# Optimization experiments

Measured on AMD Instinct MI355X. Metric: run time of the kernel, lower is better.

The kernel has to match this reference:

```python
import jax, jax.numpy as jnp
import numpy as np

N_NODES = 8192
N_EDGES = 262144
IN_DIM = 256
HID = 256
OUT_DIM = 64
PATH_DIM = 64
N_HEADS = 4


def setup_inputs() -> dict:
    key = jax.random.key(0)
    ks = jax.random.split(key, 16)
    s = 0.05
    x = jax.random.normal(ks[0], (N_NODES, IN_DIM), dtype=jnp.float32)
    edge_index = jax.random.randint(ks[1], (2, N_EDGES), 0, N_NODES, dtype=jnp.int32)
    return {
        "x": x,
        "edge_index": edge_index,
        # pathway encoder Linear(IN_DIM, PATH_DIM)
        "pe_w": jax.random.normal(ks[2], (IN_DIM, PATH_DIM), jnp.float32) * s,
        "pe_b": jax.random.normal(ks[3], (PATH_DIM,), jnp.float32) * s,
        # MultiheadAttention packed in-proj [3E, E] and out-proj [E, E]
        "in_proj_w": jax.random.normal(ks[4], (3 * PATH_DIM, PATH_DIM), jnp.float32) * s,
        "in_proj_b": jax.random.normal(ks[5], (3 * PATH_DIM,), jnp.float32) * s,
        "out_proj_w": jax.random.normal(ks[6], (PATH_DIM, PATH_DIM), jnp.float32) * s,
        "out_proj_b": jax.random.normal(ks[7], (PATH_DIM,), jnp.float32) * s,
        # GCN layer weights (in_dim, out_dim) + bias
        "w1": jax.random.normal(ks[8], (IN_DIM + PATH_DIM, HID), jnp.float32) * s,
        "b1": jax.random.normal(ks[9], (HID,), jnp.float32) * s,
        "w2": jax.random.normal(ks[10], (HID, HID), jnp.float32) * s,
        "b2": jax.random.normal(ks[11], (HID,), jnp.float32) * s,
        "w3": jax.random.normal(ks[12], (HID, OUT_DIM), jnp.float32) * s,
        "b3": jax.random.normal(ks[13], (OUT_DIM,), jnp.float32) * s,
    }


def mha_self(x, in_proj_w, in_proj_b, out_proj_w, out_proj_b):
    # unbatched nn.MultiheadAttention: x [N, E], Q=K=V=x
    N, E = x.shape
    dh = E // N_HEADS
    qkv = x @ in_proj_w.T + in_proj_b  # [N, 3E]
    q, k, v = jnp.split(qkv, 3, axis=-1)
    # [H, N, dh]
    q = q.reshape(N, N_HEADS, dh).transpose(1, 0, 2)
    k = k.reshape(N, N_HEADS, dh).transpose(1, 0, 2)
    v = v.reshape(N, N_HEADS, dh).transpose(1, 0, 2)
    scores = jnp.einsum('hnd,hmd->hnm', q, k) / jnp.sqrt(jnp.float32(dh))
    attn = jax.nn.softmax(scores, axis=-1)
    out = jnp.einsum('hnm,hmd->hnd', attn, v)  # [H, N, dh]
    out = out.transpose(1, 0, 2).reshape(N, E)
    return out @ out_proj_w.T + out_proj_b


def gcn_conv(h, edge_index, w, b, num_nodes):
    # PyG GCNConv: add self loops, symmetric normalization, linear, scatter-add, bias
    src = jnp.concatenate([edge_index[0], jnp.arange(num_nodes, dtype=edge_index.dtype)])
    dst = jnp.concatenate([edge_index[1], jnp.arange(num_nodes, dtype=edge_index.dtype)])
    deg = jax.ops.segment_sum(jnp.ones_like(dst, dtype=h.dtype), dst, num_segments=num_nodes)
    dinv = jnp.where(deg > 0, jax.lax.rsqrt(jnp.maximum(deg, 1e-12)), 0.0)
    hw = h @ w  # [N, out]
    norm = (dinv[src] * dinv[dst])[:, None]
    msg = hw[src] * norm
    out = jax.ops.segment_sum(msg, dst, num_segments=num_nodes)
    return out + b


def reference(x, edge_index, pe_w, pe_b, in_proj_w, in_proj_b, out_proj_w, out_proj_b,
              w1, b1, w2, b2, w3, b3):
    N = x.shape[0]
    pf = x @ pe_w + pe_b  # pathway encoder
    pa = mha_self(pf, in_proj_w, in_proj_b, out_proj_w, out_proj_b)
    h = jnp.concatenate([x, pa], axis=-1)  # [N, IN_DIM + PATH_DIM]
    h = jax.nn.relu(gcn_conv(h, edge_index, w1, b1, N))  # dropout is identity (eval)
    h = jax.nn.relu(gcn_conv(h, edge_index, w2, b2, N))
    h = gcn_conv(h, edge_index, w3, b3, N)
    return h
```

## Files before the change

kernel.cpp:

```cpp
#include <hip/hip_runtime.h>
#include <hip/hip_bf16.h>

#define N_NODES 8192
#define N_EDGES 262144
#define IN_DIM 256
#define HID 256
#define OUT_DIM 64
#define PATH_DIM 64
#define NHEADS 4
#define DH 16
#define KSPLIT 8
#define SPLIT_KEYS (N_NODES / KSPLIT)
#define NITER (SPLIT_KEYS / 64)

typedef __attribute__((ext_vector_type(8))) short bf16x8;
typedef __attribute__((ext_vector_type(4))) short bf16x4;
typedef __attribute__((ext_vector_type(4))) float f32x4;

__device__ __forceinline__ ushort f2bf(float f) {
  union { float f; unsigned int u; } c;
  c.f = f;
  unsigned int u = c.u;
  u += 0x7fffu + ((u >> 16) & 1u);
  return (ushort)(u >> 16);
}

__device__ __forceinline__ float bf2f(ushort u) {
  union { float f; unsigned int u; } c;
  c.u = ((unsigned int)u) << 16;
  return c.f;
}

__device__ __forceinline__ float fast_exp2(float x) {
  float r;
  asm("v_exp_f32 %0, %1" : "=v"(r) : "v"(x));
  return r;
}

__device__ __forceinline__ unsigned pack_bf16(float a, float b) {
  union { __hip_bfloat162 h; unsigned u; } c;
  c.h = __float22bfloat162_rn(make_float2(a, b));
  return c.u;
}

#if __has_builtin(__builtin_amdgcn_mfma_f32_16x16x16bf16_1k)
__device__ __forceinline__ f32x4 mfma16(bf16x4 a, bf16x4 b, f32x4 c) {
  return __builtin_amdgcn_mfma_f32_16x16x16bf16_1k(a, b, c, 0, 0, 0);
}
#else
__device__ __forceinline__ f32x4 mfma16(bf16x4 a, bf16x4 b, f32x4 c) {
  f32x4 d;
  asm volatile("v_mfma_f32_16x16x16_bf16 %0, %1, %2, %3\n\ts_nop 7\n\ts_nop 3"
               : "=v"(d) : "v"(a), "v"(b), "v"(c));
  return d;
}
#endif


__global__ __launch_bounds__(256) void init_graph(int* deg, int* cursor) {
  int i = blockIdx.x * 256 + threadIdx.x;
  if (i < N_NODES) { deg[i] = 1; cursor[i] = 0; }
}

__global__ __launch_bounds__(256) void count_deg(const int* __restrict__ dst,
                                                 int* __restrict__ deg) {
  int e = blockIdx.x * 256 + threadIdx.x;
  if (e < N_EDGES) atomicAdd(&deg[dst[e]], 1);
}

__global__ __launch_bounds__(256) void scan_rows(const int* __restrict__ deg,
                                                 int* __restrict__ row_off,
                                                 float* __restrict__ dinv) {
  __shared__ int part[256];
  int t = threadIdx.x;
  int base = t * 32;
  int local[32];
  int s = 0;
  #pragma unroll
  for (int i = 0; i < 32; ++i) {
    int c = deg[base + i] - 1;
    local[i] = s;
    s += c;
  }
  part[t] = s;
  __syncthreads();
  for (int d = 1; d < 256; d <<= 1) {
    int v = (t >= d) ? part[t - d] : 0;
    __syncthreads();
    part[t] += v;
    __syncthreads();
  }
  int prev = (t == 0) ? 0 : part[t - 1];
  #pragma unroll
  for (int i = 0; i < 32; ++i) {
    row_off[base + i] = prev + local[i];
    dinv[base + i] = rsqrtf((float)deg[base + i]);
  }
}

__global__ __launch_bounds__(256) void fill_csr(const int* __restrict__ src,
                                                const int* __restrict__ dst,
                                                const int* __restrict__ row_off,
                                                int* __restrict__ cursor,
                                                int* __restrict__ csr) {
  int e = blockIdx.x * 256 + threadIdx.x;
  if (e < N_EDGES) {
    int d = dst[e];
    int p = atomicAdd(&cursor[d], 1);
    csr[row_off[d] + p] = src[e];
  }
}


__global__ __launch_bounds__(256) void prep(const float* __restrict__ x,
                                            const float* __restrict__ pe_w,
                                            const float* __restrict__ pe_b,
                                            const float* __restrict__ in_proj_w,
                                            const float* __restrict__ in_proj_b,
                                            const float* __restrict__ out_proj_w,
                                            const float* __restrict__ w1,
                                            const float* __restrict__ w2,
                                            const float* __restrict__ w3,
                                            ushort* __restrict__ Axpa,
                                            float* __restrict__ Wpp,
                                            float* __restrict__ bpp,
                                            float* __restrict__ WtO,
                                            ushort* __restrict__ Bt1hi, ushort* __restrict__ Bt1lo,
                                            ushort* __restrict__ Bt2hi, ushort* __restrict__ Bt2lo,
                                            ushort* __restrict__ Bt3hi, ushort* __restrict__ Bt3lo) {
  const float SC = 0.36067376022224085f;
  const int b = blockIdx.x;
  const int t = threadIdx.x;
  if (b < 2048) {
    int e = b * 256 + t;
    int n = e >> 6, qi = (e & 63) << 2;
    float4 v = *reinterpret_cast<const float4*>(x + (size_t)n * 256 + qi);
    *reinterpret_cast<ushort4*>(Axpa + (size_t)n * 320 + qi) =
        make_ushort4(f2bf(v.x), f2bf(v.y), f2bf(v.z), f2bf(v.w));
  } else if (b < 2240) {
    int e = (b - 2048) * 256 + t;
    int k = e / 192, c = e % 192;
    float s = 0.f;
    for (int j = 0; j < 64; ++j) s += pe_w[k * 64 + j] * in_proj_w[c * 64 + j];
    if (c < 64) s *= SC;
    Wpp[k * 192 + c] = s;
  } else if (b == 2240) {
    if (t < 192) {
      float s = 0.f;
      for (int j = 0; j < 64; ++j) s += pe_b[j] * in_proj_w[t * 64 + j];
      s += in_proj_b[t];
      if (t < 64) s *= SC;
      bpp[t] = s;
    }
  } else if (b < 2257) {
    int e = (b - 2241) * 256 + t;
    int r = e >> 6, c = e & 63;
    WtO[c * 64 + r] = out_proj_w[e];
  } else if (b < 2577) {
    int e = (b - 2257) * 256 + t;
    int k = e >> 8, n = e & 255;
    float v = w1[e];
    ushort hi = f2bf(v);
    Bt1hi[(size_t)n * 320 + k] = hi;
    Bt1lo[(size_t)n * 320 + k] = f2bf(v - bf2f(hi));
  } else if (b < 2833) {
    int e = (b - 2577) * 256 + t;
    int k = e >> 8, n = e & 255;
    float v = w2[e];
    ushort hi = f2bf(v);
    Bt2hi[(size_t)n * 256 + k] = hi;
    Bt2lo[(size_t)n * 256 + k] = f2bf(v - bf2f(hi));
  } else {
    int e = (b - 2833) * 256 + t;
    int k = e >> 6, n = e & 63;
    float v = w3[e];
    ushort hi = f2bf(v);
    Bt3hi[(size_t)n * 256 + k] = hi;
    Bt3lo[(size_t)n * 256 + k] = f2bf(v - bf2f(hi));
  }
}


__global__ __launch_bounds__(256) void gemm_qkv(const float* __restrict__ x,
                                                const float* __restrict__ Wpp,
                                                const float* __restrict__ bpp,
                                                ushort* __restrict__ Qbf,
                                                ushort* __restrict__ Kbf,
                                                ushort* __restrict__ Vtb) {
  __shared__ __align__(16) float As[16][64];
  __shared__ __align__(16) float Bs[16][68];
  const int bm = blockIdx.y * 64;
  const int bx = blockIdx.x;
  const int bn = bx * 64;
  const int t = threadIdx.x;
  const int tx = t & 15, ty = t >> 4;
  const int am = t >> 2, ak = (t & 3) << 2;
  const int bk = t >> 4, bn4 = (t & 15) << 2;
  float acc[4][4] = {};
  for (int k0 = 0; k0 < 256; k0 += 16) {
    float4 av = *reinterpret_cast<const float4*>(x + (size_t)(bm + am) * 256 + k0 + ak);
    As[ak + 0][am] = av.x; As[ak + 1][am] = av.y;
    As[ak + 2][am] = av.z; As[ak + 3][am] = av.w;
    float4 bv = *reinterpret_cast<const float4*>(Wpp + (size_t)(k0 + bk) * 192 + bn + bn4);
    *reinterpret_cast<float4*>(&Bs[bk][bn4]) = bv;
    __syncthreads();
    #pragma unroll
    for (int k = 0; k < 16; ++k) {
      float4 a = *reinterpret_cast<const float4*>(&As[k][ty << 2]);
      float4 b = *reinterpret_cast<const float4*>(&Bs[k][tx << 2]);
      acc[0][0] += a.x * b.x; acc[0][1] += a.x * b.y; acc[0][2] += a.x * b.z; acc[0][3] += a.x * b.w;
      acc[1][0] += a.y * b.x; acc[1][1] += a.y * b.y; acc[1][2] += a.y * b.z; acc[1][3] += a.y * b.w;
      acc[2][0] += a.z * b.x; acc[2][1] += a.z * b.y; acc[2][2] += a.z * b.z; acc[2][3] += a.z * b.w;
      acc[3][0] += a.w * b.x; acc[3][1] += a.w * b.y; acc[3][2] += a.w * b.z; acc[3][3] += a.w * b.w;
    }
    __syncthreads();
  }
  const int cl = tx << 2;
  const int h = cl >> 4, d = cl & 15;
  float4 bb = *reinterpret_cast<const float4*>(bpp + bn + cl);
  const ushort4 zz = make_ushort4(0, 0, 0, 0);
  #pragma unroll
  for (int i = 0; i < 4; ++i) {
    int row = bm + (ty << 2) + i;
    float o0 = acc[i][0] + bb.x, o1 = acc[i][1] + bb.y;
    float o2 = acc[i][2] + bb.z, o3 = acc[i][3] + bb.w;
    ushort4 u = make_ushort4(f2bf(o0), f2bf(o1), f2bf(o2), f2bf(o3));
    if (bx == 0) {
      *reinterpret_cast<ushort4*>(Qbf + ((size_t)h * 8192 + row) * 32 + d) = u;
      *reinterpret_cast<ushort4*>(Qbf + ((size_t)h * 8192 + row) * 32 + d + 16) = zz;
    } else if (bx == 1) {
      *reinterpret_cast<ushort4*>(Kbf + ((size_t)h * 8192 + row) * 32 + d) = u;
      *reinterpret_cast<ushort4*>(Kbf + ((size_t)h * 8192 + row) * 32 + d + 16) = zz;
    } else {
      Vtb[((size_t)h * 16 + d + 0) * 8192 + row] = u.x;
      Vtb[((size_t)h * 16 + d + 1) * 8192 + row] = u.y;
      Vtb[((size_t)h * 16 + d + 2) * 8192 + row] = u.z;
      Vtb[((size_t)h * 16 + d + 3) * 8192 + row] = u.w;
    }
  }
}


__global__ __launch_bounds__(256) void attn_mfma5(const ushort* __restrict__ Qbf,
                                                  const ushort* __restrict__ Kbf,
                                                  const ushort* __restrict__ Vtb,
                                                  float* __restrict__ Opart,
                                                  float* __restrict__ Wpart) {
  const int h  = blockIdx.y;
  const int qb = blockIdx.x;
  const int kz = blockIdx.z;
  const int t  = threadIdx.x;
  const int wv = t >> 6;
  const int l  = t & 63;
  const int lg = l >> 4;
  const int lc = l & 15;

  __shared__ float red_o[3][64][17];
  __shared__ float red_w[3][64];

  bf16x8 qf[4];
  {
    const ushort* qbase = Qbf + ((size_t)h * 8192 + qb * 64) * 32;
    #pragma unroll
    for (int qt = 0; qt < 4; ++qt)
      qf[qt] = *reinterpret_cast<const bf16x8*>(qbase + (qt * 16 + lc) * 32 + lg * 8);
  }

  const ushort* kptr =
      Kbf + ((size_t)h * 8192 + kz * SPLIT_KEYS + wv * 16 + lc) * 32 + lg * 8;
  const ushort* vptr =
      Vtb + ((size_t)h * 16 + lc) * 8192 + kz * SPLIT_KEYS + wv * 16 + lg * 4;

  f32x4 oacc[4] = {{0.f, 0.f, 0.f, 0.f}, {0.f, 0.f, 0.f, 0.f},
                   {0.f, 0.f, 0.f, 0.f}, {0.f, 0.f, 0.f, 0.f}};
  float wsum[4] = {0.f, 0.f, 0.f, 0.f};

  bf16x8 kf = *reinterpret_cast<const bf16x8*>(kptr);
  bf16x4 vf = *reinterpret_cast<const bf16x4*>(vptr);

  for (int c = 0; c < NITER; ++c) {
    bf16x8 kf_n;
    bf16x4 vf_n;
    if (c + 1 < NITER) {
      kf_n = *reinterpret_cast<const bf16x8*>(kptr + (size_t)(c + 1) * 64 * 32);
      vf_n = *reinterpret_cast<const bf16x4*>(vptr + (size_t)(c + 1) * 64);
    }

    f32x4 s[4];
    #pragma unroll
    for (int qt = 0; qt < 4; ++qt) {
      f32x4 z = {0.f, 0.f, 0.f, 0.f};
      s[qt] = __builtin_amdgcn_mfma_f32_16x16x32_bf16(kf, qf[qt], z, 0, 0, 0);
    }

    #pragma unroll
    for (int qt = 0; qt < 4; ++qt) {
      float e0 = fast_exp2(s[qt][0]);
      float e1 = fast_exp2(s[qt][1]);
      float e2 = fast_exp2(s[qt][2]);
      float e3 = fast_exp2(s[qt][3]);
      wsum[qt] += (e0 + e1) + (e2 + e3);
      union { uint2 u; bf16x4 v; } pu;
      pu.u.x = pack_bf16(e0, e1);
      pu.u.y = pack_bf16(e2, e3);
      oacc[qt] = mfma16(pu.v, vf, oacc[qt]);
    }

    kf = kf_n;
    vf = vf_n;
  }

  #pragma unroll
  for (int qt = 0; qt < 4; ++qt) {
    float v = wsum[qt];
    v += __shfl_xor(v, 16);
    v += __shfl_xor(v, 32);
    wsum[qt] = v;
  }

  if (wv > 0) {
    #pragma unroll
    for (int qt = 0; qt < 4; ++qt) {
      #pragma unroll
      for (int r = 0; r < 4; ++r)
        red_o[wv - 1][qt * 16 + lg * 4 + r][lc] = oacc[qt][r];
      if (lg == 0) red_w[wv - 1][qt * 16 + lc] = wsum[qt];
    }
  }
  __syncthreads();

  if (wv == 0) {
    const size_t obase = ((size_t)(kz * NHEADS + h) * N_NODES + qb * 64);
    #pragma unroll
    for (int qt = 0; qt < 4; ++qt) {
      #pragma unroll
      for (int r = 0; r < 4; ++r) {
        const int q = qt * 16 + lg * 4 + r;
        float o = oacc[qt][r] + red_o[0][q][lc] + red_o[1][q][lc] + red_o[2][q][lc];
        Opart[(obase + q) * 16 + lc] = o;
      }
      if (lg == 0) {
        const int q = qt * 16 + lc;
        Wpart[obase + q] = wsum[qt] + red_w[0][q] + red_w[1][q] + red_w[2][q];
      }
    }
  }
}


__global__ __launch_bounds__(256) void gemm_pa(const float* __restrict__ Opart,
                                               const float* __restrict__ Wpart,
                                               const float* __restrict__ WtO,
                                               const float* __restrict__ ob,
                                               ushort* __restrict__ Axpa) {
  __shared__ __align__(16) float As[16][64];
  __shared__ __align__(16) float Bs[16][68];
  const int bm = blockIdx.y * 64;
  const int t = threadIdx.x;
  const int tx = t & 15, ty = t >> 4;
  const int am = t >> 2, ak = (t & 3) << 2;
  const int bk = t >> 4, bn4 = (t & 15) << 2;
  float acc[4][4] = {};
  for (int k0 = 0; k0 < 64; k0 += 16) {
    const int kk = k0 + ak;
    const int row = bm + am;
    const int h = kk >> 4, d = kk & 15;
    float ax = 0.f, ay = 0.f, az = 0.f, aw = 0.f, ws = 0.f;
    #pragma unroll
    for (int s = 0; s < KSPLIT; ++s) {
      const size_t rb = (size_t)(s * NHEADS + h) * N_NODES + row;
      float4 v = *reinterpret_cast<const float4*>(Opart + rb * 16 + d);
      ax += v.x; ay += v.y; az += v.z; aw += v.w;
      ws += Wpart[rb];
    }
    float inv = 1.f / ws;
    As[ak + 0][am] = ax * inv; As[ak + 1][am] = ay * inv;
    As[ak + 2][am] = az * inv; As[ak + 3][am] = aw * inv;
    float4 bv = *reinterpret_cast<const float4*>(WtO + (size_t)(k0 + bk) * 64 + bn4);
    *reinterpret_cast<float4*>(&Bs[bk][bn4]) = bv;
    __syncthreads();
    #pragma unroll
    for (int k = 0; k < 16; ++k) {
      float4 a = *reinterpret_cast<const float4*>(&As[k][ty << 2]);
      float4 b = *reinterpret_cast<const float4*>(&Bs[k][tx << 2]);
      acc[0][0] += a.x * b.x; acc[0][1] += a.x * b.y; acc[0][2] += a.x * b.z; acc[0][3] += a.x * b.w;
      acc[1][0] += a.y * b.x; acc[1][1] += a.y * b.y; acc[1][2] += a.y * b.z; acc[1][3] += a.y * b.w;
      acc[2][0] += a.z * b.x; acc[2][1] += a.z * b.y; acc[2][2] += a.z * b.z; acc[2][3] += a.z * b.w;
      acc[3][0] += a.w * b.x; acc[3][1] += a.w * b.y; acc[3][2] += a.w * b.z; acc[3][3] += a.w * b.w;
    }
    __syncthreads();
  }
  float4 bb = *reinterpret_cast<const float4*>(ob + (tx << 2));
  #pragma unroll
  for (int i = 0; i < 4; ++i) {
    int row = bm + (ty << 2) + i;
    float o0 = acc[i][0] + bb.x, o1 = acc[i][1] + bb.y;
    float o2 = acc[i][2] + bb.z, o3 = acc[i][3] + bb.w;
    *reinterpret_cast<ushort4*>(Axpa + (size_t)row * 320 + 256 + (tx << 2)) =
        make_ushort4(f2bf(o0), f2bf(o1), f2bf(o2), f2bf(o3));
  }
}


template <int K, int NT>
__global__ __launch_bounds__(256) void gemm_mfma(const ushort* __restrict__ A,
                                                 const ushort* __restrict__ Bthi,
                                                 const ushort* __restrict__ Btlo,
                                                 ushort* __restrict__ C) {
  const int t = threadIdx.x;
  const int wv = t >> 6;
  const int l = t & 63;
  const int lg = l >> 4;
  const int lc = l & 15;
  const int bm = blockIdx.y * 64;
  const int n = blockIdx.x * 64 + wv * 16 + lc;

  const ushort* ap = A + (size_t)(bm + lc) * K + lg * 8;
  const ushort* bh = Bthi + (size_t)n * K + lg * 8;
  const ushort* bl = Btlo + (size_t)n * K + lg * 8;

  f32x4 acc[4] = {{0.f,0.f,0.f,0.f},{0.f,0.f,0.f,0.f},{0.f,0.f,0.f,0.f},{0.f,0.f,0.f,0.f}};
  #pragma unroll 2
  for (int k0 = 0; k0 < K; k0 += 32) {
    bf16x8 vh = *reinterpret_cast<const bf16x8*>(bh + k0);
    bf16x8 vl = *reinterpret_cast<const bf16x8*>(bl + k0);
    #pragma unroll
    for (int mt = 0; mt < 4; ++mt) {
      bf16x8 af = *reinterpret_cast<const bf16x8*>(ap + (size_t)mt * 16 * K + k0);
      acc[mt] = __builtin_amdgcn_mfma_f32_16x16x32_bf16(af, vh, acc[mt], 0, 0, 0);
      acc[mt] = __builtin_amdgcn_mfma_f32_16x16x32_bf16(af, vl, acc[mt], 0, 0, 0);
    }
  }
  #pragma unroll
  for (int mt = 0; mt < 4; ++mt) {
    #pragma unroll
    for (int r = 0; r < 4; ++r)
      C[(size_t)(bm + mt * 16 + lg * 4 + r) * NT + n] = f2bf(acc[mt][r]);
  }
}


template <bool RELU>
__global__ __launch_bounds__(256) void aggregate_bf(const ushort* __restrict__ hwb,
                                                    const int* __restrict__ csr,
                                                    const int* __restrict__ row_off,
                                                    const int* __restrict__ deg,
                                                    const float* __restrict__ dinv,
                                                    const float* __restrict__ bias,
                                                    ushort* __restrict__ outb) {
  __shared__ __align__(16) float part[2][256];
  const int t = threadIdx.x;
  const int rw = t >> 7;
  const int wh = (t >> 6) & 1;
  const int l = t & 63;
  const int r = blockIdx.x * 2 + rw;
  const float dr = dinv[r];
  const int off = row_off[r];
  const int cnt = deg[r] - 1;
  const int c = l << 2;

  float a0, a1, a2, a3;
  if (wh == 0) {
    ushort4 u = *reinterpret_cast<const ushort4*>(hwb + (size_t)r * 256 + c);
    a0 = dr * bf2f(u.x); a1 = dr * bf2f(u.y); a2 = dr * bf2f(u.z); a3 = dr * bf2f(u.w);
  } else {
    a0 = a1 = a2 = a3 = 0.f;
  }
  for (int e = wh; e < cnt; e += 2) {
    int s = csr[off + e];
    float wsc = dinv[s];
    ushort4 u = *reinterpret_cast<const ushort4*>(hwb + (size_t)s * 256 + c);
    a0 += wsc * bf2f(u.x); a1 += wsc * bf2f(u.y);
    a2 += wsc * bf2f(u.z); a3 += wsc * bf2f(u.w);
  }
  if (wh == 1)
    *reinterpret_cast<float4*>(&part[rw][c]) = make_float4(a0, a1, a2, a3);
  __syncthreads();
  if (wh == 0) {
    float4 p = *reinterpret_cast<const float4*>(&part[rw][c]);
    float4 bv = *reinterpret_cast<const float4*>(bias + c);
    float o0 = dr * (a0 + p.x) + bv.x;
    float o1 = dr * (a1 + p.y) + bv.y;
    float o2 = dr * (a2 + p.z) + bv.z;
    float o3 = dr * (a3 + p.w) + bv.w;
    if (RELU) {
      o0 = fmaxf(o0, 0.f); o1 = fmaxf(o1, 0.f);
      o2 = fmaxf(o2, 0.f); o3 = fmaxf(o3, 0.f);
    }
    *reinterpret_cast<ushort4*>(outb + (size_t)r * 256 + c) =
        make_ushort4(f2bf(o0), f2bf(o1), f2bf(o2), f2bf(o3));
  }
}

__global__ __launch_bounds__(256) void aggregate64_bf(const ushort* __restrict__ hwb,
                                                      const int* __restrict__ csr,
                                                      const int* __restrict__ row_off,
                                                      const int* __restrict__ deg,
                                                      const float* __restrict__ dinv,
                                                      const float* __restrict__ bias,
                                                      float* __restrict__ out) {
  const int w = threadIdx.x >> 6, l = threadIdx.x & 63;
  const int r = blockIdx.x * 4 + w;
  const float dr = dinv[r];
  const int off = row_off[r];
  const int cnt = deg[r] - 1;
  float a = dr * bf2f(hwb[(size_t)r * 64 + l]);
  for (int e = 0; e < cnt; ++e) {
    int s = csr[off + e];
    a += dinv[s] * bf2f(hwb[(size_t)s * 64 + l]);
  }
  out[(size_t)r * 64 + l] = dr * a + bias[l];
}


extern "C" void kernel_launch(void* const* d_in, const int* in_sizes, int n_in,
                              void* d_out, int out_size, void* d_ws, size_t ws_size,
                              hipStream_t stream) {
  const float* x          = (const float*)d_in[0];
  const int*   ei         = (const int*)d_in[1];
  const float* pe_w       = (const float*)d_in[2];
  const float* pe_b       = (const float*)d_in[3];
  const float* in_proj_w  = (const float*)d_in[4];
  const float* in_proj_b  = (const float*)d_in[5];
  const float* out_proj_w = (const float*)d_in[6];
  const float* out_proj_b = (const float*)d_in[7];
  const float* w1         = (const float*)d_in[8];
  const float* b1         = (const float*)d_in[9];
  const float* w2         = (const float*)d_in[10];
  const float* b2         = (const float*)d_in[11];
  const float* w3         = (const float*)d_in[12];
  const float* b3         = (const float*)d_in[13];

  const int* esrc = ei;
  const int* edst = ei + N_EDGES;

  char* ws = (char*)d_ws;
  size_t o = 0;
  auto take = [&](size_t n) {
    char* p = ws + o;
    o += (n + 255) & ~(size_t)255;
    return p;
  };
  char*   region1 = take(18874368);
  ushort* Axpa    = (ushort*)take((size_t)N_NODES * 320 * 2);
  ushort* Qbf     = (ushort*)take((size_t)NHEADS * N_NODES * 32 * 2);
  ushort* Kbf     = (ushort*)take((size_t)NHEADS * N_NODES * 32 * 2);
  ushort* Vtb     = (ushort*)take((size_t)NHEADS * DH * N_NODES * 2);
  float*  Wpp     = (float*)take((size_t)256 * 192 * 4);
  float*  bpp     = (float*)take((size_t)192 * 4);
  float*  WtO     = (float*)take((size_t)64 * 64 * 4);
  ushort* Bt1hi   = (ushort*)take((size_t)HID * 320 * 2);
  ushort* Bt1lo   = (ushort*)take((size_t)HID * 320 * 2);
  ushort* Bt2hi   = (ushort*)take((size_t)HID * HID * 2);
  ushort* Bt2lo   = (ushort*)take((size_t)HID * HID * 2);
  ushort* Bt3hi   = (ushort*)take((size_t)OUT_DIM * HID * 2);
  ushort* Bt3lo   = (ushort*)take((size_t)OUT_DIM * HID * 2);
  float*  dinv    = (float*)take((size_t)N_NODES * 4);
  int*    deg     = (int*)take((size_t)N_NODES * 4);
  int*    cursor  = (int*)take((size_t)N_NODES * 4);
  int*    row_off = (int*)take((size_t)N_NODES * 4);
  int*    csr     = (int*)take((size_t)N_EDGES * 4);

  float* Opart = (float*)region1;
  float* Wpart = (float*)(region1 + 16777216);
  ushort* hwbf = (ushort*)region1;
  ushort* h1bf = hwbf + (size_t)N_NODES * 256;
  ushort* h2bf = h1bf + (size_t)N_NODES * 256;
  ushort* hw64 = h2bf + (size_t)N_NODES * 256;

  init_graph<<<N_NODES / 256, 256, 0, stream>>>(deg, cursor);
  count_deg<<<N_EDGES / 256, 256, 0, stream>>>(edst, deg);
  scan_rows<<<1, 256, 0, stream>>>(deg, row_off, dinv);
  fill_csr<<<N_EDGES / 256, 256, 0, stream>>>(esrc, edst, row_off, cursor, csr);

  prep<<<2897, 256, 0, stream>>>(x, pe_w, pe_b, in_proj_w, in_proj_b, out_proj_w,
                                 w1, w2, w3, Axpa, Wpp, bpp, WtO,
                                 Bt1hi, Bt1lo, Bt2hi, Bt2lo, Bt3hi, Bt3lo);

  gemm_qkv<<<dim3(3, 128), 256, 0, stream>>>(x, Wpp, bpp, Qbf, Kbf, Vtb);
  attn_mfma5<<<dim3(128, 4, KSPLIT), 256, 0, stream>>>(Qbf, Kbf, Vtb, Opart, Wpart);
  gemm_pa<<<dim3(1, 128), 256, 0, stream>>>(Opart, Wpart, WtO, out_proj_b, Axpa);

  gemm_mfma<320, 256><<<dim3(4, 128), 256, 0, stream>>>(Axpa, Bt1hi, Bt1lo, hwbf);
  aggregate_bf<true><<<N_NODES / 2, 256, 0, stream>>>(hwbf, csr, row_off, deg, dinv, b1, h1bf);
  gemm_mfma<256, 256><<<dim3(4, 128), 256, 0, stream>>>(h1bf, Bt2hi, Bt2lo, hwbf);
  aggregate_bf<true><<<N_NODES / 2, 256, 0, stream>>>(hwbf, csr, row_off, deg, dinv, b2, h2bf);
  gemm_mfma<256, 64><<<dim3(1, 128), 256, 0, stream>>>(h2bf, Bt3hi, Bt3lo, hw64);
  aggregate64_bf<<<N_NODES / 4, 256, 0, stream>>>(hw64, csr, row_off, deg, dinv, b3, (float*)d_out);
}
```

Before: 279.2 us.

## Fold attention out-projection into layer-1 weights, merge init into prep, widen aggregation

```diff
diff --git a/kernel.cpp b/kernel.cpp
--- a/kernel.cpp
+++ b/kernel.cpp
@@ -56,11 +56,6 @@
 }
 #endif
 
-
-__global__ __launch_bounds__(256) void init_graph(int* deg, int* cursor) {
-  int i = blockIdx.x * 256 + threadIdx.x;
-  if (i < N_NODES) { deg[i] = 1; cursor[i] = 0; }
-}
 
 __global__ __launch_bounds__(256) void count_deg(const int* __restrict__ dst,
                                                  int* __restrict__ deg) {
@@ -118,13 +113,16 @@
                                             const float* __restrict__ in_proj_w,
                                             const float* __restrict__ in_proj_b,
                                             const float* __restrict__ out_proj_w,
+                                            const float* __restrict__ ob,
                                             const float* __restrict__ w1,
                                             const float* __restrict__ w2,
                                             const float* __restrict__ w3,
                                             ushort* __restrict__ Axpa,
                                             float* __restrict__ Wpp,
                                             float* __restrict__ bpp,
-                                            float* __restrict__ WtO,
+                                            float* __restrict__ crow,
+                                            int* __restrict__ deg,
+                                            int* __restrict__ cursor,
                                             ushort* __restrict__ Bt1hi, ushort* __restrict__ Bt1lo,
                                             ushort* __restrict__ Bt2hi, ushort* __restrict__ Bt2lo,
                                             ushort* __restrict__ Bt3hi, ushort* __restrict__ Bt3lo) {
@@ -152,26 +150,39 @@
       if (t < 64) s *= SC;
       bpp[t] = s;
     }
-  } else if (b < 2257) {
+  } else if (b < 2305) {
     int e = (b - 2241) * 256 + t;
-    int r = e >> 6, c = e & 63;
-    WtO[c * 64 + r] = out_proj_w[e];
-  } else if (b < 2577) {
-    int e = (b - 2257) * 256 + t;
+    int d = e >> 8, m = e & 255;
+    float s = 0.f;
+    for (int c = 0; c < 64; ++c)
+      s += out_proj_w[c * 64 + d] * w1[(size_t)(256 + c) * 256 + m];
+    ushort hi = f2bf(s);
+    Bt1hi[(size_t)m * 320 + 256 + d] = hi;
+    Bt1lo[(size_t)m * 320 + 256 + d] = f2bf(s - bf2f(hi));
+  } else if (b == 2305) {
+    float s = 0.f;
+    for (int c = 0; c < 64; ++c) s += ob[c] * w1[(size_t)(256 + c) * 256 + t];
+    crow[t] = s;
+  } else if (b < 2338) {
+    int i = (b - 2306) * 256 + t;
+    deg[i] = 1;
+    cursor[i] = 0;
+  } else if (b < 2594) {
+    int e = (b - 2338) * 256 + t;
     int k = e >> 8, n = e & 255;
     float v = w1[e];
     ushort hi = f2bf(v);
     Bt1hi[(size_t)n * 320 + k] = hi;
     Bt1lo[(size_t)n * 320 + k] = f2bf(v - bf2f(hi));
-  } else if (b < 2833) {
-    int e = (b - 2577) * 256 + t;
+  } else if (b < 2850) {
+    int e = (b - 2594) * 256 + t;
     int k = e >> 8, n = e & 255;
     float v = w2[e];
     ushort hi = f2bf(v);
     Bt2hi[(size_t)n * 256 + k] = hi;
     Bt2lo[(size_t)n * 256 + k] = f2bf(v - bf2f(hi));
   } else {
-    int e = (b - 2833) * 256 + t;
+    int e = (b - 2850) * 256 + t;
     int k = e >> 6, n = e & 63;
     float v = w3[e];
     ushort hi = f2bf(v);
@@ -347,65 +358,35 @@
   }
 }
 
-
-__global__ __launch_bounds__(256) void gemm_pa(const float* __restrict__ Opart,
-                                               const float* __restrict__ Wpart,
-                                               const float* __restrict__ WtO,
-                                               const float* __restrict__ ob,
-                                               ushort* __restrict__ Axpa) {
-  __shared__ __align__(16) float As[16][64];
-  __shared__ __align__(16) float Bs[16][68];
-  const int bm = blockIdx.y * 64;
-  const int t = threadIdx.x;
-  const int tx = t & 15, ty = t >> 4;
-  const int am = t >> 2, ak = (t & 3) << 2;
-  const int bk = t >> 4, bn4 = (t & 15) << 2;
-  float acc[4][4] = {};
-  for (int k0 = 0; k0 < 64; k0 += 16) {
-    const int kk = k0 + ak;
-    const int row = bm + am;
-    const int h = kk >> 4, d = kk & 15;
-    float ax = 0.f, ay = 0.f, az = 0.f, aw = 0.f, ws = 0.f;
-    #pragma unroll
-    for (int s = 0; s < KSPLIT; ++s) {
-      const size_t rb = (size_t)(s * NHEADS + h) * N_NODES + row;
-      float4 v = *reinterpret_cast<const float4*>(Opart + rb * 16 + d);
-      ax += v.x; ay += v.y; az += v.z; aw += v.w;
-      ws += Wpart[rb];
-    }
-    float inv = 1.f / ws;
-    As[ak + 0][am] = ax * inv; As[ak + 1][am] = ay * inv;
-    As[ak + 2][am] = az * inv; As[ak + 3][am] = aw * inv;
-    float4 bv = *reinterpret_cast<const float4*>(WtO + (size_t)(k0 + bk) * 64 + bn4);
-    *reinterpret_cast<float4*>(&Bs[bk][bn4]) = bv;
-    __syncthreads();
-    #pragma unroll
-    for (int k = 0; k < 16; ++k) {
-      float4 a = *reinterpret_cast<const float4*>(&As[k][ty << 2]);
-      float4 b = *reinterpret_cast<const float4*>(&Bs[k][tx << 2]);
-      acc[0][0] += a.x * b.x; acc[0][1] += a.x * b.y; acc[0][2] += a.x * b.z; acc[0][3] += a.x * b.w;
-      acc[1][0] += a.y * b.x; acc[1][1] += a.y * b.y; acc[1][2] += a.y * b.z; acc[1][3] += a.y * b.w;
-      acc[2][0] += a.z * b.x; acc[2][1] += a.z * b.y; acc[2][2] += a.z * b.z; acc[2][3] += a.z * b.w;
-      acc[3][0] += a.w * b.x; acc[3][1] += a.w * b.y; acc[3][2] += a.w * b.z; acc[3][3] += a.w * b.w;
-    }
-    __syncthreads();
-  }
-  float4 bb = *reinterpret_cast<const float4*>(ob + (tx << 2));
+__global__ __launch_bounds__(256) void attn_combine_bf(const float* __restrict__ Opart,
+                                                       const float* __restrict__ Wpart,
+                                                       ushort* __restrict__ Axpa) {
+  int i = blockIdx.x * 256 + threadIdx.x;
+  int dq = i & 3;
+  int hn = i >> 2;
+  int h = hn >> 13;
+  int n = hn & 8191;
+  float4 acc = make_float4(0.f, 0.f, 0.f, 0.f);
+  float ws = 0.f;
   #pragma unroll
-  for (int i = 0; i < 4; ++i) {
-    int row = bm + (ty << 2) + i;
-    float o0 = acc[i][0] + bb.x, o1 = acc[i][1] + bb.y;
-    float o2 = acc[i][2] + bb.z, o3 = acc[i][3] + bb.w;
-    *reinterpret_cast<ushort4*>(Axpa + (size_t)row * 320 + 256 + (tx << 2)) =
-        make_ushort4(f2bf(o0), f2bf(o1), f2bf(o2), f2bf(o3));
-  }
-}
-
-
-template <int K, int NT>
+  for (int s = 0; s < KSPLIT; ++s) {
+    const size_t row = ((size_t)(s * NHEADS + h) * N_NODES + n);
+    float4 v = *reinterpret_cast<const float4*>(Opart + row * 16 + dq * 4);
+    acc.x += v.x; acc.y += v.y; acc.z += v.z; acc.w += v.w;
+    ws += Wpart[row];
+  }
+  float inv = 1.f / ws;
+  *reinterpret_cast<ushort4*>(Axpa + (size_t)n * 320 + 256 + h * 16 + dq * 4) =
+      make_ushort4(f2bf(acc.x * inv), f2bf(acc.y * inv),
+                   f2bf(acc.z * inv), f2bf(acc.w * inv));
+}
+
+
+template <int K, int NT, bool CROW>
 __global__ __launch_bounds__(256) void gemm_mfma(const ushort* __restrict__ A,
                                                  const ushort* __restrict__ Bthi,
                                                  const ushort* __restrict__ Btlo,
+                                                 const float* __restrict__ crow,
                                                  ushort* __restrict__ C) {
   const int t = threadIdx.x;
   const int wv = t >> 6;
@@ -431,58 +412,60 @@
       acc[mt] = __builtin_amdgcn_mfma_f32_16x16x32_bf16(af, vl, acc[mt], 0, 0, 0);
     }
   }
+  const float cr = CROW ? crow[n] : 0.f;
   #pragma unroll
   for (int mt = 0; mt < 4; ++mt) {
     #pragma unroll
     for (int r = 0; r < 4; ++r)
-      C[(size_t)(bm + mt * 16 + lg * 4 + r) * NT + n] = f2bf(acc[mt][r]);
+      C[(size_t)(bm + mt * 16 + lg * 4 + r) * NT + n] = f2bf(acc[mt][r] + cr);
   }
 }
 
 
 template <bool RELU>
-__global__ __launch_bounds__(256) void aggregate_bf(const ushort* __restrict__ hwb,
-                                                    const int* __restrict__ csr,
-                                                    const int* __restrict__ row_off,
-                                                    const int* __restrict__ deg,
-                                                    const float* __restrict__ dinv,
-                                                    const float* __restrict__ bias,
-                                                    ushort* __restrict__ outb) {
-  __shared__ __align__(16) float part[2][256];
+__global__ __launch_bounds__(256) void aggregate4_bf(const ushort* __restrict__ hwb,
+                                                     const int* __restrict__ csr,
+                                                     const int* __restrict__ row_off,
+                                                     const int* __restrict__ deg,
+                                                     const float* __restrict__ dinv,
+                                                     const float* __restrict__ bias,
+                                                     ushort* __restrict__ outb) {
+  __shared__ __align__(16) float part[3][256];
   const int t = threadIdx.x;
-  const int rw = t >> 7;
-  const int wh = (t >> 6) & 1;
+  const int wv = t >> 6;
   const int l = t & 63;
-  const int r = blockIdx.x * 2 + rw;
+  const int r = blockIdx.x;
   const float dr = dinv[r];
   const int off = row_off[r];
   const int cnt = deg[r] - 1;
   const int c = l << 2;
 
   float a0, a1, a2, a3;
-  if (wh == 0) {
+  if (wv == 0) {
     ushort4 u = *reinterpret_cast<const ushort4*>(hwb + (size_t)r * 256 + c);
     a0 = dr * bf2f(u.x); a1 = dr * bf2f(u.y); a2 = dr * bf2f(u.z); a3 = dr * bf2f(u.w);
   } else {
     a0 = a1 = a2 = a3 = 0.f;
   }
-  for (int e = wh; e < cnt; e += 2) {
+  for (int e = wv; e < cnt; e += 4) {
     int s = csr[off + e];
     float wsc = dinv[s];
     ushort4 u = *reinterpret_cast<const ushort4*>(hwb + (size_t)s * 256 + c);
     a0 += wsc * bf2f(u.x); a1 += wsc * bf2f(u.y);
     a2 += wsc * bf2f(u.z); a3 += wsc * bf2f(u.w);
   }
-  if (wh == 1)
-    *reinterpret_cast<float4*>(&part[rw][c]) = make_float4(a0, a1, a2, a3);
+  if (wv > 0)
+    *reinterpret_cast<float4*>(&part[wv - 1][c]) = make_float4(a0, a1, a2, a3);
   __syncthreads();
-  if (wh == 0) {
-    float4 p = *reinterpret_cast<const float4*>(&part[rw][c]);
+  if (wv == 0) {
+    float4 p0 = *reinterpret_cast<const float4*>(&part[0][c]);
+    float4 p1 = *reinterpret_cast<const float4*>(&part[1][c]);
+    float4 p2 = *reinterpret_cast<const float4*>(&part[2][c]);
     float4 bv = *reinterpret_cast<const float4*>(bias + c);
-    float o0 = dr * (a0 + p.x) + bv.x;
-    float o1 = dr * (a1 + p.y) + bv.y;
-    float o2 = dr * (a2 + p.z) + bv.z;
-    float o3 = dr * (a3 + p.w) + bv.w;
+    float o0 = dr * (a0 + p0.x + p1.x + p2.x) + bv.x;
+    float o1 = dr * (a1 + p0.y + p1.y + p2.y) + bv.y;
+    float o2 = dr * (a2 + p0.z + p1.z + p2.z) + bv.z;
+    float o3 = dr * (a3 + p0.w + p1.w + p2.w) + bv.w;
     if (RELU) {
       o0 = fmaxf(o0, 0.f); o1 = fmaxf(o1, 0.f);
       o2 = fmaxf(o2, 0.f); o3 = fmaxf(o3, 0.f);
@@ -548,7 +531,7 @@
   ushort* Vtb     = (ushort*)take((size_t)NHEADS * DH * N_NODES * 2);
   float*  Wpp     = (float*)take((size_t)256 * 192 * 4);
   float*  bpp     = (float*)take((size_t)192 * 4);
-  float*  WtO     = (float*)take((size_t)64 * 64 * 4);
+  float*  crow    = (float*)take((size_t)256 * 4);
   ushort* Bt1hi   = (ushort*)take((size_t)HID * 320 * 2);
   ushort* Bt1lo   = (ushort*)take((size_t)HID * 320 * 2);
   ushort* Bt2hi   = (ushort*)take((size_t)HID * HID * 2);
@@ -568,23 +551,23 @@
   ushort* h2bf = h1bf + (size_t)N_NODES * 256;
   ushort* hw64 = h2bf + (size_t)N_NODES * 256;
 
-  init_graph<<<N_NODES / 256, 256, 0, stream>>>(deg, cursor);
+  prep<<<2914, 256, 0, stream>>>(x, pe_w, pe_b, in_proj_w, in_proj_b, out_proj_w,
+                                 out_proj_b, w1, w2, w3, Axpa, Wpp, bpp, crow,
+                                 deg, cursor,
+                                 Bt1hi, Bt1lo, Bt2hi, Bt2lo, Bt3hi, Bt3lo);
+
   count_deg<<<N_EDGES / 256, 256, 0, stream>>>(edst, deg);
   scan_rows<<<1, 256, 0, stream>>>(deg, row_off, dinv);
   fill_csr<<<N_EDGES / 256, 256, 0, stream>>>(esrc, edst, row_off, cursor, csr);
 
-  prep<<<2897, 256, 0, stream>>>(x, pe_w, pe_b, in_proj_w, in_proj_b, out_proj_w,
-                                 w1, w2, w3, Axpa, Wpp, bpp, WtO,
-                                 Bt1hi, Bt1lo, Bt2hi, Bt2lo, Bt3hi, Bt3lo);
-
   gemm_qkv<<<dim3(3, 128), 256, 0, stream>>>(x, Wpp, bpp, Qbf, Kbf, Vtb);
   attn_mfma5<<<dim3(128, 4, KSPLIT), 256, 0, stream>>>(Qbf, Kbf, Vtb, Opart, Wpart);
-  gemm_pa<<<dim3(1, 128), 256, 0, stream>>>(Opart, Wpart, WtO, out_proj_b, Axpa);
-
-  gemm_mfma<320, 256><<<dim3(4, 128), 256, 0, stream>>>(Axpa, Bt1hi, Bt1lo, hwbf);
-  aggregate_bf<true><<<N_NODES / 2, 256, 0, stream>>>(hwbf, csr, row_off, deg, dinv, b1, h1bf);
-  gemm_mfma<256, 256><<<dim3(4, 128), 256, 0, stream>>>(h1bf, Bt2hi, Bt2lo, hwbf);
-  aggregate_bf<true><<<N_NODES / 2, 256, 0, stream>>>(hwbf, csr, row_off, deg, dinv, b2, h2bf);
-  gemm_mfma<256, 64><<<dim3(1, 128), 256, 0, stream>>>(h2bf, Bt3hi, Bt3lo, hw64);
+  attn_combine_bf<<<(NHEADS * N_NODES * 4) / 256, 256, 0, stream>>>(Opart, Wpart, Axpa);
+
+  gemm_mfma<320, 256, true><<<dim3(4, 128), 256, 0, stream>>>(Axpa, Bt1hi, Bt1lo, crow, hwbf);
+  aggregate4_bf<true><<<N_NODES, 256, 0, stream>>>(hwbf, csr, row_off, deg, dinv, b1, h1bf);
+  gemm_mfma<256, 256, false><<<dim3(4, 128), 256, 0, stream>>>(h1bf, Bt2hi, Bt2lo, nullptr, hwbf);
+  aggregate4_bf<true><<<N_NODES, 256, 0, stream>>>(hwbf, csr, row_off, deg, dinv, b2, h2bf);
+  gemm_mfma<256, 64, false><<<dim3(1, 128), 256, 0, stream>>>(h2bf, Bt3hi, Bt3lo, nullptr, hw64);
   aggregate64_bf<<<N_NODES / 4, 256, 0, stream>>>(hw64, csr, row_off, deg, dinv, b3, (float*)d_out);
 }
```

Result: faster. 271.2 us (-2.8%).
